# Kernel tuning notes

Measured on AMD Instinct MI355X. Metric: run time of the kernel, lower is better.

## Reference

```python
import jax, jax.numpy as jnp
import numpy as np

EMBED_DIM = 768
NUM_HEADS = 12
HEAD_DIM = EMBED_DIM // NUM_HEADS


def setup_inputs() -> dict:
    key = jax.random.key(0)
    ks = jax.random.split(key, 6)
    B, N = 8, 1024
    x = jax.random.normal(ks[0], (B, N, EMBED_DIM), dtype=jnp.float32)
    pos_embedding = jax.random.normal(ks[1], (1, NUM_HEADS, N, N), dtype=jnp.float32)
    s_in = 1.0 / np.sqrt(EMBED_DIM)
    W_qkv = jax.random.normal(ks[2], (EMBED_DIM, 3 * EMBED_DIM), dtype=jnp.float32) * s_in
    b_qkv = jnp.zeros((3 * EMBED_DIM,), dtype=jnp.float32)
    W_proj = jax.random.normal(ks[3], (EMBED_DIM, EMBED_DIM), dtype=jnp.float32) * s_in
    b_proj = jnp.zeros((EMBED_DIM,), dtype=jnp.float32)
    return {"x": x, "pos_embedding": pos_embedding, "W_qkv": W_qkv,
            "b_qkv": b_qkv, "W_proj": W_proj, "b_proj": b_proj}


def reference(x, pos_embedding, W_qkv, b_qkv, W_proj, b_proj):
    B, N, C = x.shape
    H, D = NUM_HEADS, HEAD_DIM
    qkv = x @ W_qkv + b_qkv                      # [B,N,3C]
    qkv = qkv.reshape(B, N, 3, H, D)
    q = qkv[:, :, 0].transpose(0, 2, 1, 3)       # [B,H,N,D]
    k = qkv[:, :, 1].transpose(0, 2, 1, 3)
    v = qkv[:, :, 2].transpose(0, 2, 1, 3)
    # NOTE: bias is added BEFORE scaling, matching the original module.
    scores = (jnp.einsum('bhnd,bhmd->bhnm', q, k) + pos_embedding) / jnp.sqrt(
        jnp.asarray(D, dtype=x.dtype))
    attn = jax.nn.softmax(scores, axis=-1)       # dropout is identity in eval
    out = jnp.einsum('bhnm,bhmd->bhnd', attn, v)
    out = out.transpose(0, 2, 1, 3).reshape(B, N, C)
    return out @ W_proj + b_proj
```

## Files before the change

kernel.cpp:

```cpp
#include <hip/hip_runtime.h>

#define SEQ   1024
#define HEADS 12
#define CDIM  768
#define BATCH 8

#define QSCALE 0.18033688011112042f

typedef __attribute__((ext_vector_type(8))) short bf16x8;
typedef __attribute__((ext_vector_type(4))) float f32x4;
typedef __attribute__((ext_vector_type(16))) float f32x16;
typedef __attribute__((ext_vector_type(4))) float float4v;
typedef __attribute__((ext_vector_type(4))) short short4v;

__device__ __forceinline__ void gload_lds16(const void* g, void* l) {
  __builtin_amdgcn_global_load_lds(
      (const __attribute__((address_space(1))) unsigned int*)g,
      (__attribute__((address_space(3))) unsigned int*)l, 16, 0, 0);
}

__device__ __forceinline__ unsigned short f2bf(float f) {
  union { float f; unsigned u; } v; v.f = f;
  unsigned r = v.u + 0x7fff + ((v.u >> 16) & 1);
  return (unsigned short)(r >> 16);
}

__device__ __forceinline__ unsigned cvtpk(float a, float b) {
  unsigned r;
  asm("v_cvt_pk_bf16_f32 %0, %1, %2" : "=v"(r) : "v"(a), "v"(b));
  return r;
}

__device__ __forceinline__ float bfsel(unsigned u, int odd) {
  union { unsigned u; float f; } v;
  v.u = odd ? (u & 0xffff0000u) : (u << 16);
  return v.f;
}

__global__ __launch_bounds__(256) void prep_x_kernel(const float* __restrict__ x,
                                                     short* __restrict__ A) {
  int i = blockIdx.x * 256 + threadIdx.x;
  int r = i / 192;
  int c4 = (i % 192) * 4;
  float4v xv = *(const float4v*)(x + (size_t)r * 768 + c4);
  short4v hi;
#pragma unroll
  for (int j = 0; j < 4; ++j) hi[j] = (short)f2bf(xv[j]);
  *(short4v*)(A + (size_t)r * 768 + c4) = hi;
}

__global__ __launch_bounds__(256) void prep_w_kernel(const float* __restrict__ W,
                                                     short* __restrict__ Bt) {
  __shared__ float tile[64][65];
  int k0 = blockIdx.x * 64;
  int n0 = blockIdx.y * 64;
  int t = threadIdx.x;
#pragma unroll
  for (int it = 0; it < 16; ++it) {
    int r = it * 4 + (t >> 6);
    int c = t & 63;
    tile[r][c] = W[(size_t)(k0 + r) * 2304 + n0 + c];
  }
  __syncthreads();
#pragma unroll
  for (int it = 0; it < 16; ++it) {
    int nr = it * 4 + (t >> 6);
    int kc = t & 63;
    Bt[(size_t)(n0 + nr) * 768 + k0 + kc] = (short)f2bf(tile[kc][nr]);
  }
}

__global__ __launch_bounds__(256) void prep_wp_kernel(const float* __restrict__ W,
                                                      short* __restrict__ Bt) {
  __shared__ float tile[64][65];
  int k0 = blockIdx.x * 64;
  int n0 = blockIdx.y * 64;
  int t = threadIdx.x;
#pragma unroll
  for (int it = 0; it < 16; ++it) {
    int r = it * 4 + (t >> 6);
    int c = t & 63;
    tile[r][c] = W[(size_t)(k0 + r) * 768 + n0 + c];
  }
  __syncthreads();
#pragma unroll
  for (int it = 0; it < 16; ++it) {
    int nr = it * 4 + (t >> 6);
    int kc = t & 63;
    Bt[(size_t)(n0 + nr) * 768 + k0 + kc] = (short)f2bf(tile[kc][nr]);
  }
}

__global__ __launch_bounds__(256) void prep_pos_kernel(const float* __restrict__ P,
                                                       short* __restrict__ PB) {
  int t = blockIdx.x * 256 + threadIdx.x;
  int lane = t & 63;
  int jh   = (t >> 6) & 1;
  int i0   = (t >> 7) & 1;
  int w    = (t >> 8) & 3;
  int ti   = (t >> 10) & 15;
  int qblk = (t >> 14) & 7;
  int h    = t >> 17;
  int c5 = lane & 31, g1 = lane >> 5;
  int q = qblk * 128 + w * 32 + c5;
  const float* src = P + ((size_t)h * SEQ + q) * SEQ
                     + ti * 64 + i0 * 32 + 4 * g1 + 16 * jh;
  float4v v0 = *(const float4v*)(src);
  float4v v1 = *(const float4v*)(src + 8);
  union { short s[8]; bf16x8 v; } o;
#pragma unroll
  for (int p = 0; p < 4; ++p) {
    o.s[p]     = (short)f2bf(v0[p] * QSCALE);
    o.s[4 + p] = (short)f2bf(v1[p] * QSCALE);
  }
  *(bf16x8*)(PB + (size_t)t * 8) = o.v;
}

template <int MODE>
__global__ __launch_bounds__(512, 4) void gemm_kernel(
    const short* __restrict__ A, const short* __restrict__ Bt,
    const float* __restrict__ bias,
    short* __restrict__ outQ, short* __restrict__ outK, short* __restrict__ outVT,
    float* __restrict__ outF) {
  constexpr int NBLK = (MODE == 1) ? 18 : 6;
  constexpr int CHUNK = (MODE == 1) ? 144 : 48;
  const int bid = blockIdx.x;
  const int lb = (bid & 7) * CHUNK + (bid >> 3);
  const int n0 = (lb % NBLK) * 128;
  const int m0 = (lb / NBLK) * 128;

  __shared__ short Als[2][128 * 64];
  __shared__ short Bls[2][128 * 64];
  const int tid = threadIdx.x;
  const int lane = tid & 63;
  const int w = tid >> 6;
  const int wr = (w & 1) * 64;
  const int wc = (w >> 1) * 32;
  f32x4 acc[4][2];
#pragma unroll
  for (int mi = 0; mi < 4; ++mi)
#pragma unroll
    for (int ni = 0; ni < 2; ++ni) acc[mi][ni] = (f32x4){0.f, 0.f, 0.f, 0.f};

  auto STAGE = [&](int buf, int k0) {
#pragma unroll
    for (int pass = 0; pass < 2; ++pass) {
      int rbase = pass * 64 + w * 8;
      int row = rbase + (lane >> 3);
      int ul = (lane & 7) ^ (row & 7);
      gload_lds16(A + (size_t)(m0 + row) * 768 + k0 + ul * 8, Als[buf] + rbase * 64);
      gload_lds16(Bt + (size_t)(n0 + row) * 768 + k0 + ul * 8, Bls[buf] + rbase * 64);
    }
  };

  STAGE(0, 0);
  asm volatile("s_waitcnt vmcnt(0)" ::: "memory");
  __builtin_amdgcn_sched_barrier(0);
  __builtin_amdgcn_s_barrier();

  for (int t = 0; t < 12; ++t) {
    if (t < 11) STAGE((t + 1) & 1, (t + 1) * 64);
    const short* Ab = Als[t & 1];
    const short* Bb = Bls[t & 1];
    __builtin_amdgcn_s_setprio(1);
#pragma unroll
    for (int kk = 0; kk < 2; ++kk) {
      bf16x8 af[4], bfv[2];
#pragma unroll
      for (int mi = 0; mi < 4; ++mi) {
        int row = wr + mi * 16 + (lane & 15);
        int off = (row * 128 + kk * 64 + (lane >> 4) * 16) ^ ((row & 7) << 4);
        af[mi] = *(const bf16x8*)((const char*)Ab + off);
      }
#pragma unroll
      for (int ni = 0; ni < 2; ++ni) {
        int row = wc + ni * 16 + (lane & 15);
        int off = (row * 128 + kk * 64 + (lane >> 4) * 16) ^ ((row & 7) << 4);
        bfv[ni] = *(const bf16x8*)((const char*)Bb + off);
      }
#pragma unroll
      for (int mi = 0; mi < 4; ++mi)
#pragma unroll
        for (int ni = 0; ni < 2; ++ni)
          acc[mi][ni] = __builtin_amdgcn_mfma_f32_16x16x32_bf16(
              af[mi], bfv[ni], acc[mi][ni], 0, 0, 0);
    }
    __builtin_amdgcn_s_setprio(0);
    if (t < 11) {
      asm volatile("s_waitcnt vmcnt(0)" ::: "memory");
      __builtin_amdgcn_sched_barrier(0);
      __builtin_amdgcn_s_barrier();
    }
  }

  if (MODE == 1) {
    const int three = n0 / 768;
    const int nb = n0 - three * 768;
#pragma unroll
    for (int mi = 0; mi < 4; ++mi)
#pragma unroll
      for (int ni = 0; ni < 2; ++ni)
#pragma unroll
        for (int j = 0; j < 4; ++j) {
          int row = m0 + wr + mi * 16 + ((lane >> 4) << 2) + j;
          int col = n0 + wc + ni * 16 + (lane & 15);
          float v = acc[mi][ni][j] + bias[col];
          int rem = nb + wc + ni * 16 + (lane & 15);
          int hh = rem >> 6, d = rem & 63;
          int b = row >> 10, n = row & 1023;
          size_t bh = (size_t)(b * 12 + hh);
          if (three == 0)      outQ[(bh * 1024 + n) * 64 + d] = (short)f2bf(v * QSCALE);
          else if (three == 1) outK[(bh * 1024 + n) * 64 + d] = (short)f2bf(v);
          else                 outVT[(bh * 64 + d) * 1024 + n] = (short)f2bf(v);
        }
  } else {
#pragma unroll
    for (int mi = 0; mi < 4; ++mi)
#pragma unroll
      for (int ni = 0; ni < 2; ++ni)
#pragma unroll
        for (int j = 0; j < 4; ++j) {
          int row = m0 + wr + mi * 16 + ((lane >> 4) << 2) + j;
          int col = n0 + wc + ni * 16 + (lane & 15);
          outF[(size_t)row * 768 + col] = acc[mi][ni][j] + bias[col];
        }
  }
}

#define MKFRAG(B, pA, pB, pC, pD)                                    \
  { unsigned x0 = (pA), y0 = (pC), x1 = (pB), y1 = (pD);             \
    asm("v_permlane32_swap_b32 %0, %1" : "+v"(x0), "+v"(y0));        \
    asm("v_permlane32_swap_b32 %0, %1" : "+v"(x1), "+v"(y1));        \
    B.u[0] = x0; B.u[1] = x1; B.u[2] = y0; B.u[3] = y1; }

__global__ __launch_bounds__(256, 3) void attn_kernel(
    const short* __restrict__ qb, const short* __restrict__ kb,
    const short* __restrict__ vtb, const short* __restrict__ posb,
    short* __restrict__ outb) {
  const int bid = blockIdx.x;
  const int lb = (bid & 7) * 96 + (bid >> 3);
  const int qblk = lb & 7;
  const int hb = lb >> 3;
  const int h = hb >> 3, b = hb & 7;

  const int tid = threadIdx.x, lane = tid & 63, w = tid >> 6;
  const int c5 = lane & 31, g1 = lane >> 5;
  const size_t bh = (size_t)(b * 12 + h);
  const short* Q = qb + bh * SEQ * 64;
  const short* K = kb + bh * SEQ * 64;
  const short* VT = vtb + bh * 64 * SEQ;
  const int q0w = qblk * 128 + w * 32;

  const short* pwb = posb + (size_t)h * 1048576 + (size_t)qblk * 131072
                     + w * 2048 + lane * 8;

  __shared__ short kls[3 * 4096];
  __shared__ short vls[3 * 4096];

  bf16x8 qf[4];
#pragma unroll
  for (int kd = 0; kd < 4; ++kd)
    qf[kd] = *(const bf16x8*)(Q + (size_t)(q0w + c5) * 64 + kd * 16 + g1 * 8);

  f32x16 o0, o1;
#pragma unroll
  for (int i = 0; i < 16; ++i) { o0[i] = 0.f; o1[i] = 0.f; }
  float lsum = 0.f;

  auto STAGE = [&](short* kb_, short* vb_, int kv0) {
    int r0 = w * 8 + (lane >> 3);
    int u0 = (lane & 7) ^ (r0 & 7);
    gload_lds16(K + (size_t)(kv0 + r0) * 64 + u0 * 8, kb_ + w * 512);
    gload_lds16(K + (size_t)(kv0 + 32 + r0) * 64 + u0 * 8, kb_ + 2048 + w * 512);
    gload_lds16(VT + (size_t)r0 * SEQ + kv0 + u0 * 8, vb_ + w * 512);
    gload_lds16(VT + (size_t)(32 + r0) * SEQ + kv0 + u0 * 8, vb_ + 2048 + w * 512);
  };

  short* kbuf0 = kls;        short* vbuf0 = vls;
  short* kbuf1 = kls + 4096; short* vbuf1 = vls + 4096;
  short* kbuf2 = kls + 8192; short* vbuf2 = vls + 8192;

  STAGE(kbuf0, vbuf0, 0);
  STAGE(kbuf1, vbuf1, 64);
  asm volatile("s_waitcnt vmcnt(4)" ::: "memory");
  __builtin_amdgcn_sched_barrier(0);
  __builtin_amdgcn_s_barrier();

  for (int ti = 0; ti < 16; ++ti) {
    const int kv0 = ti * 64;

    union { bf16x8 v; unsigned u[4]; } ua0, ua1, ub0, ub1;
    ua0.v = *(const bf16x8*)(pwb + ti * 8192);
    ua1.v = *(const bf16x8*)(pwb + ti * 8192 + 512);
    ub0.v = *(const bf16x8*)(pwb + ti * 8192 + 1024);
    ub1.v = *(const bf16x8*)(pwb + ti * 8192 + 1536);
    asm volatile("" ::: "memory");
    if (ti < 14) STAGE(kbuf2, vbuf2, kv0 + 128);

    const short* kc = kbuf0;
    const short* vc = vbuf0;

    f32x16 p0, p1;
#pragma unroll
    for (int i = 0; i < 16; ++i) { p0[i] = 0.f; p1[i] = 0.f; }
    __builtin_amdgcn_s_setprio(1);
#pragma unroll
    for (int kd = 0; kd < 4; ++kd) {
      int off0 = (c5 * 128 + kd * 32 + g1 * 16) ^ ((c5 & 7) << 4);
      int off1 = ((32 + c5) * 128 + kd * 32 + g1 * 16) ^ ((c5 & 7) << 4);
      bf16x8 kf0 = *(const bf16x8*)((const char*)kc + off0);
      bf16x8 kf1 = *(const bf16x8*)((const char*)kc + off1);
      p0 = __builtin_amdgcn_mfma_f32_32x32x16_bf16(kf0, qf[kd], p0, 0, 0, 0);
      p1 = __builtin_amdgcn_mfma_f32_32x32x16_bf16(kf1, qf[kd], p1, 0, 0, 0);
    }
    __builtin_amdgcn_s_setprio(0);

#pragma unroll
    for (int r = 0; r < 16; ++r) {
      unsigned wa = (r < 8) ? ua0.u[(r >> 1) & 3] : ua1.u[(r >> 1) & 3];
      unsigned wb = (r < 8) ? ub0.u[(r >> 1) & 3] : ub1.u[(r >> 1) & 3];
      float a = exp2f(p0[r] + bfsel(wa, r & 1));
      float bq = exp2f(p1[r] + bfsel(wb, r & 1));
      p0[r] = a; p1[r] = bq;
      lsum += a + bq;
    }

    unsigned pk0[8], pk1[8];
#pragma unroll
    for (int m = 0; m < 4; ++m) {
      pk0[2 * m]     = cvtpk(p0[4 * m],     p0[4 * m + 1]);
      pk0[2 * m + 1] = cvtpk(p0[4 * m + 2], p0[4 * m + 3]);
      pk1[2 * m]     = cvtpk(p1[4 * m],     p1[4 * m + 1]);
      pk1[2 * m + 1] = cvtpk(p1[4 * m + 2], p1[4 * m + 3]);
    }

    union bb { bf16x8 v; unsigned u[4]; } B0, B1, B2, B3;
    MKFRAG(B0, pk0[0], pk0[1], pk0[2], pk0[3]);
    MKFRAG(B1, pk0[4], pk0[5], pk0[6], pk0[7]);
    MKFRAG(B2, pk1[0], pk1[1], pk1[2], pk1[3]);
    MKFRAG(B3, pk1[4], pk1[5], pk1[6], pk1[7]);

    __builtin_amdgcn_s_setprio(1);
#define PVSTEP(Bv, s)                                                        \
    { int o0f = (c5 * 128 + (s) * 32 + g1 * 16) ^ ((c5 & 7) << 4);           \
      int o1f = ((32 + c5) * 128 + (s) * 32 + g1 * 16) ^ ((c5 & 7) << 4);    \
      bf16x8 vf0 = *(const bf16x8*)((const char*)vc + o0f);                  \
      bf16x8 vf1 = *(const bf16x8*)((const char*)vc + o1f);                  \
      o0 = __builtin_amdgcn_mfma_f32_32x32x16_bf16(vf0, Bv.v, o0, 0, 0, 0);  \
      o1 = __builtin_amdgcn_mfma_f32_32x32x16_bf16(vf1, Bv.v, o1, 0, 0, 0); }
    PVSTEP(B0, 0); PVSTEP(B1, 1); PVSTEP(B2, 2); PVSTEP(B3, 3);
#undef PVSTEP
    __builtin_amdgcn_s_setprio(0);

    short* tk = kbuf0; kbuf0 = kbuf1; kbuf1 = kbuf2; kbuf2 = tk;
    short* tv = vbuf0; vbuf0 = vbuf1; vbuf1 = vbuf2; vbuf2 = tv;

    if (ti < 15) {
      if (ti < 14) asm volatile("s_waitcnt vmcnt(4)" ::: "memory");
      else         asm volatile("s_waitcnt vmcnt(0)" ::: "memory");
      __builtin_amdgcn_sched_barrier(0);
      __builtin_amdgcn_s_barrier();
    }
  }

  lsum += __shfl_xor(lsum, 32);
  float inv = 1.0f / lsum;
  size_t obase = (size_t)(b * SEQ + q0w + c5) * 768 + h * 64 + g1 * 4;
#pragma unroll
  for (int m = 0; m < 4; ++m) {
    short4v ov0, ov1;
#pragma unroll
    for (int j = 0; j < 4; ++j) {
      ov0[j] = (short)f2bf(o0[4 * m + j] * inv);
      ov1[j] = (short)f2bf(o1[4 * m + j] * inv);
    }
    *(short4v*)(outb + obase + m * 8) = ov0;
    *(short4v*)(outb + obase + 32 + m * 8) = ov1;
  }
}

extern "C" void kernel_launch(void* const* d_in, const int* in_sizes, int n_in,
                              void* d_out, int out_size, void* d_ws, size_t ws_size,
                              hipStream_t stream) {
  const float* x      = (const float*)d_in[0];
  const float* pos    = (const float*)d_in[1];
  const float* W_qkv  = (const float*)d_in[2];
  const float* b_qkv  = (const float*)d_in[3];
  const float* W_proj = (const float*)d_in[4];
  const float* b_proj = (const float*)d_in[5];
  float* out = (float*)d_out;

  char* ws = (char*)d_ws;
  short* A       = (short*)(ws);
  short* attnbuf = (short*)(ws);
  short* Bt      = (short*)(ws + 12582912);
  short* wpt     = (short*)(ws + 16121856);
  short* qbuf    = (short*)(ws + 17301504);
  short* kbuf    = (short*)(ws + 29884416);
  short* vtbuf   = (short*)(ws + 42467328);
  short* posb    = (short*)(ws + 55050240);

  prep_x_kernel<<<6144, 256, 0, stream>>>(x, A);
  prep_w_kernel<<<dim3(12, 36), 256, 0, stream>>>(W_qkv, Bt);
  prep_wp_kernel<<<dim3(12, 12), 256, 0, stream>>>(W_proj, wpt);
  prep_pos_kernel<<<6144, 256, 0, stream>>>(pos, posb);
  gemm_kernel<1><<<1152, 512, 0, stream>>>(A, Bt, b_qkv,
                                           qbuf, kbuf, vtbuf, nullptr);
  attn_kernel<<<768, 256, 0, stream>>>(qbuf, kbuf, vtbuf, posb, attnbuf);
  gemm_kernel<2><<<384, 512, 0, stream>>>(attnbuf, wpt, b_proj,
                                          nullptr, nullptr, nullptr, out);
}
```

Before: 152.6 us.

## Widen GEMM tiles to 128x192 and add triple-buffered LDS prefetch

The QKV and output-projection GEMMs now use 128x192 output tiles, three MFMA column fragments per wave, and a three-stage LDS ring that prefetches two k-steps ahead using partial vmcnt waits. Larger tiles raise arithmetic intensity and the deeper pipeline is meant to hide global-load latency better. In exchange the kernel uses more LDS, gets a lower occupancy bound and fewer blocks (768 and 256), which may hurt load balance across CUs. The epilogue head/QKV split still works because 768 is divisible by 192.

```diff
diff --git a/kernel.cpp b/kernel.cpp
--- a/kernel.cpp
+++ b/kernel.cpp
@@ -117,77 +117,82 @@
 }
 
 template <int MODE>
-__global__ __launch_bounds__(512, 4) void gemm_kernel(
+__global__ __launch_bounds__(512, 2) void gemm_kernel(
     const short* __restrict__ A, const short* __restrict__ Bt,
     const float* __restrict__ bias,
     short* __restrict__ outQ, short* __restrict__ outK, short* __restrict__ outVT,
     float* __restrict__ outF) {
-  constexpr int NBLK = (MODE == 1) ? 18 : 6;
-  constexpr int CHUNK = (MODE == 1) ? 144 : 48;
+  constexpr int NBLK = (MODE == 1) ? 12 : 4;
+  constexpr int CHUNK = (MODE == 1) ? 96 : 32;
   const int bid = blockIdx.x;
   const int lb = (bid & 7) * CHUNK + (bid >> 3);
-  const int n0 = (lb % NBLK) * 128;
+  const int n0 = (lb % NBLK) * 192;
   const int m0 = (lb / NBLK) * 128;
 
-  __shared__ short Als[2][128 * 64];
-  __shared__ short Bls[2][128 * 64];
+  __shared__ short lds[3 * 20480];
+
   const int tid = threadIdx.x;
   const int lane = tid & 63;
   const int w = tid >> 6;
   const int wr = (w & 1) * 64;
-  const int wc = (w >> 1) * 32;
-  f32x4 acc[4][2];
+  const int wc = (w >> 1) * 48;
+  f32x4 acc[4][3];
 #pragma unroll
   for (int mi = 0; mi < 4; ++mi)
 #pragma unroll
-    for (int ni = 0; ni < 2; ++ni) acc[mi][ni] = (f32x4){0.f, 0.f, 0.f, 0.f};
+    for (int ni = 0; ni < 3; ++ni) acc[mi][ni] = (f32x4){0.f, 0.f, 0.f, 0.f};
 
   auto STAGE = [&](int buf, int k0) {
-#pragma unroll
-    for (int pass = 0; pass < 2; ++pass) {
-      int rbase = pass * 64 + w * 8;
-      int row = rbase + (lane >> 3);
-      int ul = (lane & 7) ^ (row & 7);
-      gload_lds16(A + (size_t)(m0 + row) * 768 + k0 + ul * 8, Als[buf] + rbase * 64);
-      gload_lds16(Bt + (size_t)(n0 + row) * 768 + k0 + ul * 8, Bls[buf] + rbase * 64);
-    }
+    short* base = lds + buf * 20480;
+    int rowlow = w * 8 + (lane >> 3);
+    int ul = (lane & 7) ^ (rowlow & 7);
+#pragma unroll
+    for (int seg = 0; seg < 2; ++seg)
+      gload_lds16(A + (size_t)(m0 + seg * 64 + rowlow) * 768 + k0 + ul * 8,
+                  base + (seg * 64 + w * 8) * 64);
+#pragma unroll
+    for (int seg = 0; seg < 3; ++seg)
+      gload_lds16(Bt + (size_t)(n0 + seg * 64 + rowlow) * 768 + k0 + ul * 8,
+                  base + 8192 + (seg * 64 + w * 8) * 64);
   };
 
   STAGE(0, 0);
-  asm volatile("s_waitcnt vmcnt(0)" ::: "memory");
+  STAGE(1, 64);
+  asm volatile("s_waitcnt vmcnt(5)" ::: "memory");
   __builtin_amdgcn_sched_barrier(0);
   __builtin_amdgcn_s_barrier();
 
   for (int t = 0; t < 12; ++t) {
-    if (t < 11) STAGE((t + 1) & 1, (t + 1) * 64);
-    const short* Ab = Als[t & 1];
-    const short* Bb = Bls[t & 1];
+    if (t < 10) STAGE((t + 2) % 3, (t + 2) * 64);
+    const char* Ab = (const char*)(lds + (t % 3) * 20480);
+    const char* Bb = Ab + 16384;
     __builtin_amdgcn_s_setprio(1);
 #pragma unroll
     for (int kk = 0; kk < 2; ++kk) {
-      bf16x8 af[4], bfv[2];
+      bf16x8 af[4], bfv[3];
 #pragma unroll
       for (int mi = 0; mi < 4; ++mi) {
         int row = wr + mi * 16 + (lane & 15);
         int off = (row * 128 + kk * 64 + (lane >> 4) * 16) ^ ((row & 7) << 4);
-        af[mi] = *(const bf16x8*)((const char*)Ab + off);
+        af[mi] = *(const bf16x8*)(Ab + off);
       }
 #pragma unroll
-      for (int ni = 0; ni < 2; ++ni) {
+      for (int ni = 0; ni < 3; ++ni) {
         int row = wc + ni * 16 + (lane & 15);
         int off = (row * 128 + kk * 64 + (lane >> 4) * 16) ^ ((row & 7) << 4);
-        bfv[ni] = *(const bf16x8*)((const char*)Bb + off);
+        bfv[ni] = *(const bf16x8*)(Bb + off);
       }
 #pragma unroll
       for (int mi = 0; mi < 4; ++mi)
 #pragma unroll
-        for (int ni = 0; ni < 2; ++ni)
+        for (int ni = 0; ni < 3; ++ni)
           acc[mi][ni] = __builtin_amdgcn_mfma_f32_16x16x32_bf16(
               af[mi], bfv[ni], acc[mi][ni], 0, 0, 0);
     }
     __builtin_amdgcn_s_setprio(0);
     if (t < 11) {
-      asm volatile("s_waitcnt vmcnt(0)" ::: "memory");
+      if (t < 10) asm volatile("s_waitcnt vmcnt(5)" ::: "memory");
+      else        asm volatile("s_waitcnt vmcnt(0)" ::: "memory");
       __builtin_amdgcn_sched_barrier(0);
       __builtin_amdgcn_s_barrier();
     }
@@ -199,7 +204,7 @@
 #pragma unroll
     for (int mi = 0; mi < 4; ++mi)
 #pragma unroll
-      for (int ni = 0; ni < 2; ++ni)
+      for (int ni = 0; ni < 3; ++ni)
 #pragma unroll
         for (int j = 0; j < 4; ++j) {
           int row = m0 + wr + mi * 16 + ((lane >> 4) << 2) + j;
@@ -217,7 +222,7 @@
 #pragma unroll
     for (int mi = 0; mi < 4; ++mi)
 #pragma unroll
-      for (int ni = 0; ni < 2; ++ni)
+      for (int ni = 0; ni < 3; ++ni)
 #pragma unroll
         for (int j = 0; j < 4; ++j) {
           int row = m0 + wr + mi * 16 + ((lane >> 4) << 2) + j;
@@ -404,9 +409,9 @@
   prep_w_kernel<<<dim3(12, 36), 256, 0, stream>>>(W_qkv, Bt);
   prep_wp_kernel<<<dim3(12, 12), 256, 0, stream>>>(W_proj, wpt);
   prep_pos_kernel<<<6144, 256, 0, stream>>>(pos, posb);
-  gemm_kernel<1><<<1152, 512, 0, stream>>>(A, Bt, b_qkv,
-                                           qbuf, kbuf, vtbuf, nullptr);
+  gemm_kernel<1><<<768, 512, 0, stream>>>(A, Bt, b_qkv,
+                                          qbuf, kbuf, vtbuf, nullptr);
   attn_kernel<<<768, 256, 0, stream>>>(qbuf, kbuf, vtbuf, posb, attnbuf);
-  gemm_kernel<2><<<384, 512, 0, stream>>>(attnbuf, wpt, b_proj,
+  gemm_kernel<2><<<256, 512, 0, stream>>>(attnbuf, wpt, b_proj,
                                           nullptr, nullptr, nullptr, out);
 }
```

After: 151.7 us. About the same (-0.6%).

## Triple-buffer GEMM K-tiles at depth 32 with two-stage-ahead prefetch

Applied to the files above, without the earlier changes.

The QKV and output-projection GEMM now splits K into 24 steps of 32 instead of 12 steps of 64. It keeps three LDS buffers and issues loads two steps ahead, waiting on vmcnt(2) instead of draining all loads. This also cuts LDS per block from 64KB to 48KB and raises the launch-bounds occupancy hint from 4 to 6. The intent is to hide global-load latency and allow more resident blocks, at the cost of twice as many barriers and less MFMA work per step.

```diff
diff --git a/kernel.cpp b/kernel.cpp
--- a/kernel.cpp
+++ b/kernel.cpp
@@ -117,7 +117,7 @@
 }
 
 template <int MODE>
-__global__ __launch_bounds__(512, 4) void gemm_kernel(
+__global__ __launch_bounds__(512, 6) void gemm_kernel(
     const short* __restrict__ A, const short* __restrict__ Bt,
     const float* __restrict__ bias,
     short* __restrict__ outQ, short* __restrict__ outK, short* __restrict__ outVT,
@@ -129,13 +129,14 @@
   const int n0 = (lb % NBLK) * 128;
   const int m0 = (lb / NBLK) * 128;
 
-  __shared__ short Als[2][128 * 64];
-  __shared__ short Bls[2][128 * 64];
+  __shared__ short lds[3 * 8192];
+
   const int tid = threadIdx.x;
   const int lane = tid & 63;
   const int w = tid >> 6;
   const int wr = (w & 1) * 64;
   const int wc = (w >> 1) * 32;
+  const int c = lane & 15, g = lane >> 4;
   f32x4 acc[4][2];
 #pragma unroll
   for (int mi = 0; mi < 4; ++mi)
@@ -143,51 +144,45 @@
     for (int ni = 0; ni < 2; ++ni) acc[mi][ni] = (f32x4){0.f, 0.f, 0.f, 0.f};
 
   auto STAGE = [&](int buf, int k0) {
-#pragma unroll
-    for (int pass = 0; pass < 2; ++pass) {
-      int rbase = pass * 64 + w * 8;
-      int row = rbase + (lane >> 3);
-      int ul = (lane & 7) ^ (row & 7);
-      gload_lds16(A + (size_t)(m0 + row) * 768 + k0 + ul * 8, Als[buf] + rbase * 64);
-      gload_lds16(Bt + (size_t)(n0 + row) * 768 + k0 + ul * 8, Bls[buf] + rbase * 64);
-    }
+    short* base = lds + buf * 8192;
+    int row = tid >> 2;
+    int us = (tid & 3) ^ (row & 3);
+    gload_lds16(A + (size_t)(m0 + row) * 768 + k0 + us * 8, base + w * 512);
+    gload_lds16(Bt + (size_t)(n0 + row) * 768 + k0 + us * 8, base + 4096 + w * 512);
   };
 
   STAGE(0, 0);
-  asm volatile("s_waitcnt vmcnt(0)" ::: "memory");
+  STAGE(1, 32);
+  asm volatile("s_waitcnt vmcnt(2)" ::: "memory");
   __builtin_amdgcn_sched_barrier(0);
   __builtin_amdgcn_s_barrier();
 
-  for (int t = 0; t < 12; ++t) {
-    if (t < 11) STAGE((t + 1) & 1, (t + 1) * 64);
-    const short* Ab = Als[t & 1];
-    const short* Bb = Bls[t & 1];
+  for (int t = 0; t < 24; ++t) {
+    if (t < 22) STAGE((t + 2) % 3, (t + 2) * 32);
+    const char* Ab = (const char*)(lds + (t % 3) * 8192);
+    const char* Bb = Ab + 8192;
     __builtin_amdgcn_s_setprio(1);
-#pragma unroll
-    for (int kk = 0; kk < 2; ++kk) {
-      bf16x8 af[4], bfv[2];
-#pragma unroll
-      for (int mi = 0; mi < 4; ++mi) {
-        int row = wr + mi * 16 + (lane & 15);
-        int off = (row * 128 + kk * 64 + (lane >> 4) * 16) ^ ((row & 7) << 4);
-        af[mi] = *(const bf16x8*)((const char*)Ab + off);
-      }
-#pragma unroll
-      for (int ni = 0; ni < 2; ++ni) {
-        int row = wc + ni * 16 + (lane & 15);
-        int off = (row * 128 + kk * 64 + (lane >> 4) * 16) ^ ((row & 7) << 4);
-        bfv[ni] = *(const bf16x8*)((const char*)Bb + off);
-      }
-#pragma unroll
-      for (int mi = 0; mi < 4; ++mi)
-#pragma unroll
-        for (int ni = 0; ni < 2; ++ni)
-          acc[mi][ni] = __builtin_amdgcn_mfma_f32_16x16x32_bf16(
-              af[mi], bfv[ni], acc[mi][ni], 0, 0, 0);
-    }
+    bf16x8 af[4], bfv[2];
+#pragma unroll
+    for (int mi = 0; mi < 4; ++mi) {
+      int row = wr + mi * 16 + c;
+      af[mi] = *(const bf16x8*)(Ab + row * 64 + ((g ^ (row & 3)) * 16));
+    }
+#pragma unroll
+    for (int ni = 0; ni < 2; ++ni) {
+      int row = wc + ni * 16 + c;
+      bfv[ni] = *(const bf16x8*)(Bb + row * 64 + ((g ^ (row & 3)) * 16));
+    }
+#pragma unroll
+    for (int mi = 0; mi < 4; ++mi)
+#pragma unroll
+      for (int ni = 0; ni < 2; ++ni)
+        acc[mi][ni] = __builtin_amdgcn_mfma_f32_16x16x32_bf16(
+            af[mi], bfv[ni], acc[mi][ni], 0, 0, 0);
     __builtin_amdgcn_s_setprio(0);
-    if (t < 11) {
-      asm volatile("s_waitcnt vmcnt(0)" ::: "memory");
+    if (t < 23) {
+      if (t < 22) asm volatile("s_waitcnt vmcnt(2)" ::: "memory");
+      else        asm volatile("s_waitcnt vmcnt(0)" ::: "memory");
       __builtin_amdgcn_sched_barrier(0);
       __builtin_amdgcn_s_barrier();
     }
@@ -202,10 +197,10 @@
       for (int ni = 0; ni < 2; ++ni)
 #pragma unroll
         for (int j = 0; j < 4; ++j) {
-          int row = m0 + wr + mi * 16 + ((lane >> 4) << 2) + j;
-          int col = n0 + wc + ni * 16 + (lane & 15);
+          int row = m0 + wr + mi * 16 + (g << 2) + j;
+          int col = n0 + wc + ni * 16 + c;
           float v = acc[mi][ni][j] + bias[col];
-          int rem = nb + wc + ni * 16 + (lane & 15);
+          int rem = nb + wc + ni * 16 + c;
           int hh = rem >> 6, d = rem & 63;
           int b = row >> 10, n = row & 1023;
           size_t bh = (size_t)(b * 12 + hh);
@@ -220,8 +215,8 @@
       for (int ni = 0; ni < 2; ++ni)
 #pragma unroll
         for (int j = 0; j < 4; ++j) {
-          int row = m0 + wr + mi * 16 + ((lane >> 4) << 2) + j;
-          int col = n0 + wc + ni * 16 + (lane & 15);
+          int row = m0 + wr + mi * 16 + (g << 2) + j;
+          int col = n0 + wc + ni * 16 + c;
           outF[(size_t)row * 768 + col] = acc[mi][ni][j] + bias[col];
         }
   }
```

New measurement: 153.6 us. No clear change (+0.7%).
